# Kernel optimization log

Hardware: AMD Instinct MI355X
Metric: run time of the kernel (lower is better)

The kernel has to match this reference:

```python
import jax, jax.numpy as jnp
import numpy as np

N, E, D = 50000, 300000, 64
EPS = 0.0  # eps buffer, train_eps=False


def setup_inputs() -> dict:
    key = jax.random.key(0)
    ks = jax.random.split(key, 24)
    inp = {}
    i = 0
    for d in range(3):
        inp[f"x{d}"] = jax.random.normal(ks[i], (N, D), jnp.float32); i += 1
        inp[f"up_index{d}"] = jax.random.randint(ks[i], (2, E), 0, N, jnp.int32); i += 1
        inp[f"down_index{d}"] = jax.random.randint(ks[i], (2, E), 0, N, jnp.int32); i += 1
        inp[f"up_attr{d}"] = jax.random.normal(ks[i], (E, D), jnp.float32); i += 1
        inp[f"down_attr{d}"] = jax.random.normal(ks[i], (E, D), jnp.float32); i += 1
    s2 = 1.0 / np.sqrt(2 * D)
    s1 = 1.0 / np.sqrt(D)
    inp["W_up"] = jax.random.normal(ks[i], (2 * D, D), jnp.float32) * s2; i += 1
    inp["b_up"] = jnp.zeros((D,), jnp.float32)
    inp["W_down"] = jax.random.normal(ks[i], (2 * D, D), jnp.float32) * s2; i += 1
    inp["b_down"] = jnp.zeros((D,), jnp.float32)
    inp["W1"] = jax.random.normal(ks[i], (D, D), jnp.float32) * s1; i += 1
    inp["b1"] = jnp.zeros((D,), jnp.float32)
    inp["W2"] = jax.random.normal(ks[i], (D, D), jnp.float32) * s1; i += 1
    inp["b2"] = jnp.zeros((D,), jnp.float32)
    return inp


def _level(x, up_idx, down_idx, up_attr, down_attr,
           W_up, b_up, W_down, b_down, W1, b1, W2, b2):
    # message_up: gather source feats, concat attr, MLP, scatter-add to targets
    m_up = jax.nn.relu(jnp.concatenate([x[up_idx[1]], up_attr], axis=-1) @ W_up + b_up)
    out_up = jax.ops.segment_sum(m_up, up_idx[0], num_segments=N)
    m_dn = jax.nn.relu(jnp.concatenate([x[down_idx[1]], down_attr], axis=-1) @ W_down + b_down)
    out_dn = jax.ops.segment_sum(m_dn, down_idx[0], num_segments=N)
    # out_up += (1+eps)x; out_down += (1+eps)x; update(out_up + out_down)
    h = out_up + out_dn + (2.0 * (1.0 + EPS)) * x
    return jax.nn.relu(jax.nn.relu(h @ W1 + b1) @ W2 + b2)


def reference(x0, up_index0, down_index0, up_attr0, down_attr0,
              x1, up_index1, down_index1, up_attr1, down_attr1,
              x2, up_index2, down_index2, up_attr2, down_attr2,
              W_up, b_up, W_down, b_down, W1, b1, W2, b2):
    params = (W_up, b_up, W_down, b_down, W1, b1, W2, b2)
    o0 = _level(x0, up_index0, down_index0, up_attr0, down_attr0, *params)
    o1 = _level(x1, up_index1, down_index1, up_attr1, down_attr1, *params)
    o2 = _level(x2, up_index2, down_index2, up_attr2, down_attr2, *params)
    return (o0, o1, o2)
```

## Files before the change

kernel.cpp:

```cpp
#include <hip/hip_runtime.h>
#include <hip/hip_fp16.h>

#define NN 50000
#define NE 300000
#define ETILES (NE / 16)
#define NTILES (NN / 16)

typedef _Float16 f16;
typedef _Float16 f16x4 __attribute__((ext_vector_type(4)));
typedef float f32x4 __attribute__((ext_vector_type(4)));

__device__ __forceinline__ f16x4 cvt4(float4 v) {
    f16x4 r; r.x = (f16)v.x; r.y = (f16)v.y; r.z = (f16)v.z; r.w = (f16)v.w;
    return r;
}

template<bool HALF>
__global__ void init_kernel(const float* __restrict__ x0, const float* __restrict__ x1,
                            const float* __restrict__ x2, void* __restrict__ hbase) {
    const size_t i = (size_t)blockIdx.x * 256 + threadIdx.x;
    const int lvl = (int)(i / (NN * 16));
    const size_t li = i - (size_t)lvl * (NN * 16);
    const float* xs = (lvl == 0) ? x0 : (lvl == 1) ? x1 : x2;
    float4 v = ((const float4*)xs)[li];
    if (HALF) {
        f16x4 o;
        o.x = (f16)(2.f * v.x); o.y = (f16)(2.f * v.y);
        o.z = (f16)(2.f * v.z); o.w = (f16)(2.f * v.w);
        ((f16x4*)((f16*)hbase + (size_t)lvl * NN * 64))[li] = o;
    } else {
        ((float4*)((float*)hbase + (size_t)lvl * NN * 64))[li] =
            make_float4(2.f * v.x, 2.f * v.y, 2.f * v.z, 2.f * v.w);
    }
}

__global__ void wtrans_kernel(const float* __restrict__ WU, const float* __restrict__ WD,
                              f16* __restrict__ WtU, f16* __restrict__ WtD) {
    const int i = blockIdx.x * 256 + threadIdx.x;
    const int k = i >> 6, c = i & 63;
    WtU[c * 128 + k] = (f16)WU[i];
    WtD[c * 128 + k] = (f16)WD[i];
}

__global__ __launch_bounds__(256) void edge2_kernel(
    const float* __restrict__ x,
    const int* __restrict__ ui, const int* __restrict__ di,
    const float* __restrict__ ua, const float* __restrict__ da,
    const f16* __restrict__ WtU, const f16* __restrict__ WtD,
    const float* __restrict__ bU, const float* __restrict__ bD,
    __half* __restrict__ h) {

    const int dir = blockIdx.y;
    const int* __restrict__ idx   = dir ? di : ui;
    const float* __restrict__ attr = dir ? da : ua;
    const f16* __restrict__ Wt    = dir ? WtD : WtU;
    const float* __restrict__ b   = dir ? bD : bU;

    const int t    = threadIdx.x;
    const int lane = t & 63;
    const int wid  = t >> 6;
    const int lr   = lane & 15;
    const int lg   = (lane >> 4) & 3;
    const int l5   = lane & 31;

    f16x4 wf[8][4];
#pragma unroll
    for (int k0 = 0; k0 < 8; ++k0)
#pragma unroll
        for (int n = 0; n < 4; ++n)
            wf[k0][n] = *(const f16x4*)&Wt[(n * 16 + lr) * 128 + k0 * 16 + 4 * lg];
    float bf[4];
#pragma unroll
    for (int n = 0; n < 4; ++n) bf[n] = b[n * 16 + lr];

    const float4* x4 = (const float4*)x;
    const float4* a4 = (const float4*)attr;

    const int gw     = blockIdx.x * 4 + wid;
    const int stride = gridDim.x * 4;

    int tile = gw;
    if (tile >= ETILES) return;

    int comb;
    float4 pA[4];
    {
        const int e0 = tile << 4;
        comb = idx[(l5 < 16) ? (NE + e0 + l5) : (e0 + l5 - 16)];
#pragma unroll
        for (int k0 = 0; k0 < 4; ++k0)
            pA[k0] = a4[(size_t)(e0 + lr) * 16 + 4 * k0 + lg];
    }

    for (; tile < ETILES; tile += stride) {
        const int src = __shfl(comb, lr);
        int tg[4];
#pragma unroll
        for (int j = 0; j < 4; ++j) tg[j] = __shfl(comb, 16 + 4 * lg + j);

        float4 gx[4];
#pragma unroll
        for (int k0 = 0; k0 < 4; ++k0)
            gx[k0] = x4[(size_t)src * 16 + 4 * k0 + lg];

        const int tn = tile + stride;
        int combN = 0;
        float4 pAn[4] = {};
        if (tn < ETILES) {
            const int e0n = tn << 4;
            combN = idx[(l5 < 16) ? (NE + e0n + l5) : (e0n + l5 - 16)];
#pragma unroll
            for (int k0 = 0; k0 < 4; ++k0)
                pAn[k0] = a4[(size_t)(e0n + lr) * 16 + 4 * k0 + lg];
        }

        f16x4 a[8];
#pragma unroll
        for (int k0 = 0; k0 < 4; ++k0) a[4 + k0] = cvt4(pA[k0]);
#pragma unroll
        for (int k0 = 0; k0 < 4; ++k0) a[k0] = cvt4(gx[k0]);

        f32x4 acc[4];
#pragma unroll
        for (int n = 0; n < 4; ++n) acc[n] = (f32x4){0.f, 0.f, 0.f, 0.f};
#pragma unroll
        for (int k0 = 0; k0 < 8; ++k0)
#pragma unroll
            for (int n = 0; n < 4; ++n)
                acc[n] = __builtin_amdgcn_mfma_f32_16x16x16f16(a[k0], wf[k0][n], acc[n], 0, 0, 0);

#pragma unroll
        for (int j = 0; j < 4; ++j) {
            float v[4], vn[4];
#pragma unroll
            for (int n = 0; n < 4; ++n) v[n] = fmaxf(acc[n][j] + bf[n], 0.f);
#pragma unroll
            for (int n = 0; n < 4; ++n) vn[n] = __shfl_xor(v[n], 1);
            __half* hp = h + (size_t)tg[j] * 64;
            if ((lane & 1) == 0) {
                unsafeAtomicAdd((__half2*)(hp + 0 * 16 + lr), __floats2half2_rn(v[0], vn[0]));
                unsafeAtomicAdd((__half2*)(hp + 1 * 16 + lr), __floats2half2_rn(v[1], vn[1]));
            } else {
                unsafeAtomicAdd((__half2*)(hp + 2 * 16 + lr - 1), __floats2half2_rn(vn[2], v[2]));
                unsafeAtomicAdd((__half2*)(hp + 3 * 16 + lr - 1), __floats2half2_rn(vn[3], v[3]));
            }
        }

        comb = combN;
#pragma unroll
        for (int k0 = 0; k0 < 4; ++k0) pA[k0] = pAn[k0];
    }
}

__global__ __launch_bounds__(256) void edge_f32_kernel(
    const float* __restrict__ x, const int* __restrict__ idx,
    const float* __restrict__ attr, const float* __restrict__ W,
    const float* __restrict__ b, float* __restrict__ h) {

    const int t    = threadIdx.x;
    const int lane = t & 63;
    const int wid  = t >> 6;
    const int lr   = lane & 15;
    const int lg   = (lane >> 4) & 3;

    f16x4 wf[8][4];
#pragma unroll
    for (int k0 = 0; k0 < 8; ++k0) {
        const int kb = k0 * 16 + 4 * lg;
#pragma unroll
        for (int n = 0; n < 4; ++n) {
            const int c = n * 16 + lr;
            f16x4 w;
            w.x = (f16)W[(kb + 0) * 64 + c];
            w.y = (f16)W[(kb + 1) * 64 + c];
            w.z = (f16)W[(kb + 2) * 64 + c];
            w.w = (f16)W[(kb + 3) * 64 + c];
            wf[k0][n] = w;
        }
    }
    float bf[4];
#pragma unroll
    for (int n = 0; n < 4; ++n) bf[n] = b[n * 16 + lr];

    const float4* x4 = (const float4*)x;
    const float4* a4 = (const float4*)attr;

    const int gw     = blockIdx.x * 4 + wid;
    const int stride = gridDim.x * 4;
    for (int tile = gw; tile < ETILES; tile += stride) {
        const int e0  = tile << 4;
        const int src = idx[NE + e0 + lr];
        int tg[4];
#pragma unroll
        for (int j = 0; j < 4; ++j) tg[j] = idx[e0 + 4 * lg + j];

        f16x4 a[8];
#pragma unroll
        for (int k0 = 0; k0 < 4; ++k0)
            a[k0] = cvt4(x4[(size_t)src * 16 + 4 * k0 + lg]);
#pragma unroll
        for (int k0 = 0; k0 < 4; ++k0)
            a[4 + k0] = cvt4(a4[(size_t)(e0 + lr) * 16 + 4 * k0 + lg]);

        f32x4 acc[4];
#pragma unroll
        for (int n = 0; n < 4; ++n) acc[n] = (f32x4){0.f, 0.f, 0.f, 0.f};
#pragma unroll
        for (int k0 = 0; k0 < 8; ++k0)
#pragma unroll
            for (int n = 0; n < 4; ++n)
                acc[n] = __builtin_amdgcn_mfma_f32_16x16x16f16(a[k0], wf[k0][n], acc[n], 0, 0, 0);

#pragma unroll
        for (int j = 0; j < 4; ++j) {
            float* hp = h + (size_t)tg[j] * 64;
#pragma unroll
            for (int n = 0; n < 4; ++n) {
                float v = fmaxf(acc[n][j] + bf[n], 0.f);
                unsafeAtomicAdd(hp + n * 16 + lr, v);
            }
        }
    }
}

template<bool HALF>
__global__ __launch_bounds__(256) void node_kernel(
    const void* __restrict__ hbase, float* __restrict__ outb,
    const float* __restrict__ W1, const float* __restrict__ b1,
    const float* __restrict__ W2, const float* __restrict__ b2) {

    __shared__ f16 Y[4][16 * 72];

    const int t    = threadIdx.x;
    const int lane = t & 63;
    const int wid  = t >> 6;
    const int lr   = lane & 15;
    const int lg   = (lane >> 4) & 3;

    f16x4 w1f[4][4], w2f[4][4];
#pragma unroll
    for (int k0 = 0; k0 < 4; ++k0) {
        const int kb = k0 * 16 + 4 * lg;
#pragma unroll
        for (int n = 0; n < 4; ++n) {
            const int c = n * 16 + lr;
            f16x4 w;
            w.x = (f16)W1[(kb + 0) * 64 + c];
            w.y = (f16)W1[(kb + 1) * 64 + c];
            w.z = (f16)W1[(kb + 2) * 64 + c];
            w.w = (f16)W1[(kb + 3) * 64 + c];
            w1f[k0][n] = w;
            w.x = (f16)W2[(kb + 0) * 64 + c];
            w.y = (f16)W2[(kb + 1) * 64 + c];
            w.z = (f16)W2[(kb + 2) * 64 + c];
            w.w = (f16)W2[(kb + 3) * 64 + c];
            w2f[k0][n] = w;
        }
    }
    float b1f[4], b2f[4];
#pragma unroll
    for (int n = 0; n < 4; ++n) {
        b1f[n] = b1[n * 16 + lr];
        b2f[n] = b2[n * 16 + lr];
    }

    const int gw     = blockIdx.x * 4 + wid;
    const int stride = gridDim.x * 4;
    for (int tile = gw; tile < 3 * NTILES; tile += stride) {
        const int lvl = tile / NTILES;
        const int n0  = (tile - lvl * NTILES) << 4;
        float* out = outb + (size_t)lvl * NN * 64;

        f16x4 a[4];
        if (HALF) {
            const f16* h16 = (const f16*)hbase + (size_t)lvl * NN * 64;
#pragma unroll
            for (int k0 = 0; k0 < 4; ++k0)
                a[k0] = *(const f16x4*)&h16[(size_t)(n0 + lr) * 64 + k0 * 16 + 4 * lg];
        } else {
            const float4* h4 = (const float4*)((const float*)hbase + (size_t)lvl * NN * 64);
#pragma unroll
            for (int k0 = 0; k0 < 4; ++k0)
                a[k0] = cvt4(h4[(size_t)(n0 + lr) * 16 + 4 * k0 + lg]);
        }

        f32x4 acc[4];
#pragma unroll
        for (int n = 0; n < 4; ++n) acc[n] = (f32x4){0.f, 0.f, 0.f, 0.f};
#pragma unroll
        for (int k0 = 0; k0 < 4; ++k0)
#pragma unroll
            for (int n = 0; n < 4; ++n)
                acc[n] = __builtin_amdgcn_mfma_f32_16x16x16f16(a[k0], w1f[k0][n], acc[n], 0, 0, 0);

#pragma unroll
        for (int n = 0; n < 4; ++n)
#pragma unroll
            for (int j = 0; j < 4; ++j) {
                float v = acc[n][j] + b1f[n];
                v = v > 0.f ? v : 0.f;
                Y[wid][(4 * lg + j) * 72 + n * 16 + lr] = (f16)v;
            }

        f16x4 a2[4];
#pragma unroll
        for (int k0 = 0; k0 < 4; ++k0)
            a2[k0] = *(const f16x4*)&Y[wid][lr * 72 + k0 * 16 + 4 * lg];

        f32x4 acc2[4];
#pragma unroll
        for (int n = 0; n < 4; ++n) acc2[n] = (f32x4){0.f, 0.f, 0.f, 0.f};
#pragma unroll
        for (int k0 = 0; k0 < 4; ++k0)
#pragma unroll
            for (int n = 0; n < 4; ++n)
                acc2[n] = __builtin_amdgcn_mfma_f32_16x16x16f16(a2[k0], w2f[k0][n], acc2[n], 0, 0, 0);

#pragma unroll
        for (int n = 0; n < 4; ++n)
#pragma unroll
            for (int j = 0; j < 4; ++j) {
                float v = acc2[n][j] + b2f[n];
                v = v > 0.f ? v : 0.f;
                out[(size_t)(n0 + 4 * lg + j) * 64 + n * 16 + lr] = v;
            }
    }
}

extern "C" void kernel_launch(void* const* d_in, const int* in_sizes, int n_in,
                              void* d_out, int out_size, void* d_ws, size_t ws_size,
                              hipStream_t stream) {
    (void)in_sizes; (void)n_in; (void)out_size;

    const float* W_up   = (const float*)d_in[15];
    const float* b_up   = (const float*)d_in[16];
    const float* W_down = (const float*)d_in[17];
    const float* b_down = (const float*)d_in[18];
    const float* W1     = (const float*)d_in[19];
    const float* b1     = (const float*)d_in[20];
    const float* W2     = (const float*)d_in[21];
    const float* b2     = (const float*)d_in[22];

    const float* x0 = (const float*)d_in[0];
    const float* x1 = (const float*)d_in[5];
    const float* x2 = (const float*)d_in[10];

    const size_t hbytes = (size_t)3 * NN * 64 * sizeof(__half);
    const bool half_ok = ws_size >= hbytes + 2 * 128 * 64 * sizeof(f16);

    if (half_ok) {
        f16* hbase = (f16*)d_ws;
        f16* WtU = (f16*)((char*)d_ws + hbytes);
        f16* WtD = WtU + 128 * 64;

        wtrans_kernel<<<32, 256, 0, stream>>>(W_up, W_down, WtU, WtD);
        init_kernel<true><<<9375, 256, 0, stream>>>(x0, x1, x2, hbase);
        for (int d = 0; d < 3; ++d) {
            const float* x  = (const float*)d_in[5 * d + 0];
            const int*   ui = (const int*)  d_in[5 * d + 1];
            const int*   di = (const int*)  d_in[5 * d + 2];
            const float* ua = (const float*)d_in[5 * d + 3];
            const float* da = (const float*)d_in[5 * d + 4];
            __half* h = (__half*)(hbase + (size_t)d * NN * 64);
            edge2_kernel<<<dim3(1024, 2), 256, 0, stream>>>(
                x, ui, di, ua, da, WtU, WtD, b_up, b_down, h);
        }
        node_kernel<true><<<586, 256, 0, stream>>>(hbase, (float*)d_out, W1, b1, W2, b2);
    } else {
        float* hbase = (float*)d_out;
        init_kernel<false><<<9375, 256, 0, stream>>>(x0, x1, x2, hbase);
        for (int d = 0; d < 3; ++d) {
            const float* x  = (const float*)d_in[5 * d + 0];
            const int*   ui = (const int*)  d_in[5 * d + 1];
            const int*   di = (const int*)  d_in[5 * d + 2];
            const float* ua = (const float*)d_in[5 * d + 3];
            const float* da = (const float*)d_in[5 * d + 4];
            float* h = hbase + (size_t)d * NN * 64;
            edge_f32_kernel<<<1024, 256, 0, stream>>>(x, ui, ua, W_up,   b_up,   h);
            edge_f32_kernel<<<1024, 256, 0, stream>>>(x, di, da, W_down, b_down, h);
        }
        node_kernel<false><<<586, 256, 0, stream>>>(hbase, (float*)d_out, W1, b1, W2, b2);
    }
}
```

Before: 443.1 us.

## Gather fp16 copy of x, move weights to LDS, deepen edge prefetch pipeline

The init kernel now also writes an fp16 copy of each level's x, so the edge kernel gathers 128 bytes per row instead of 256. Weight fragments move from 32 VGPR-resident vectors into padded shared memory, which frees registers for occupancy and costs LDS reads per MFMA. The edge loop now prefetches indices two tiles ahead and gathered rows one tile ahead. The fp16 path needs a larger workspace; if the workspace is too small the code falls back to the fp32 path.

```diff
diff --git a/kernel.cpp b/kernel.cpp
--- a/kernel.cpp
+++ b/kernel.cpp
@@ -8,6 +8,7 @@
 
 typedef _Float16 f16;
 typedef _Float16 f16x4 __attribute__((ext_vector_type(4)));
+typedef _Float16 f16x8 __attribute__((ext_vector_type(8)));
 typedef float f32x4 __attribute__((ext_vector_type(4)));
 
 __device__ __forceinline__ f16x4 cvt4(float4 v) {
@@ -15,23 +16,30 @@
     return r;
 }
 
-template<bool HALF>
-__global__ void init_kernel(const float* __restrict__ x0, const float* __restrict__ x1,
-                            const float* __restrict__ x2, void* __restrict__ hbase) {
+__global__ void init2_kernel(const float* __restrict__ x0, const float* __restrict__ x1,
+                             const float* __restrict__ x2,
+                             f16* __restrict__ hbase, f16* __restrict__ xhbase) {
     const size_t i = (size_t)blockIdx.x * 256 + threadIdx.x;
     const int lvl = (int)(i / (NN * 16));
     const size_t li = i - (size_t)lvl * (NN * 16);
     const float* xs = (lvl == 0) ? x0 : (lvl == 1) ? x1 : x2;
     float4 v = ((const float4*)xs)[li];
-    if (HALF) {
-        f16x4 o;
-        o.x = (f16)(2.f * v.x); o.y = (f16)(2.f * v.y);
-        o.z = (f16)(2.f * v.z); o.w = (f16)(2.f * v.w);
-        ((f16x4*)((f16*)hbase + (size_t)lvl * NN * 64))[li] = o;
-    } else {
-        ((float4*)((float*)hbase + (size_t)lvl * NN * 64))[li] =
-            make_float4(2.f * v.x, 2.f * v.y, 2.f * v.z, 2.f * v.w);
-    }
+    f16x4 xo, ho;
+    xo.x = (f16)v.x;        xo.y = (f16)v.y;        xo.z = (f16)v.z;        xo.w = (f16)v.w;
+    ho.x = (f16)(2.f*v.x);  ho.y = (f16)(2.f*v.y);  ho.z = (f16)(2.f*v.z);  ho.w = (f16)(2.f*v.w);
+    ((f16x4*)(xhbase + (size_t)lvl * NN * 64))[li] = xo;
+    ((f16x4*)(hbase  + (size_t)lvl * NN * 64))[li] = ho;
+}
+
+__global__ void initf32_kernel(const float* __restrict__ x0, const float* __restrict__ x1,
+                               const float* __restrict__ x2, float* __restrict__ hbase) {
+    const size_t i = (size_t)blockIdx.x * 256 + threadIdx.x;
+    const int lvl = (int)(i / (NN * 16));
+    const size_t li = i - (size_t)lvl * (NN * 16);
+    const float* xs = (lvl == 0) ? x0 : (lvl == 1) ? x1 : x2;
+    float4 v = ((const float4*)xs)[li];
+    ((float4*)(hbase + (size_t)lvl * NN * 64))[li] =
+        make_float4(2.f * v.x, 2.f * v.y, 2.f * v.z, 2.f * v.w);
 }
 
 __global__ void wtrans_kernel(const float* __restrict__ WU, const float* __restrict__ WD,
@@ -42,92 +50,112 @@
     WtD[c * 128 + k] = (f16)WD[i];
 }
 
-__global__ __launch_bounds__(256) void edge2_kernel(
-    const float* __restrict__ x,
+#define WLDS_STRIDE 136
+
+__device__ __forceinline__ int ld_comb(const int* __restrict__ idx, int tile, int l5) {
+    const int e0 = tile << 4;
+    return idx[(l5 < 16) ? (NE + e0 + l5) : (e0 + l5 - 16)];
+}
+
+__global__ __launch_bounds__(256) void edge4_kernel(
+    const f16* __restrict__ xh,
     const int* __restrict__ ui, const int* __restrict__ di,
     const float* __restrict__ ua, const float* __restrict__ da,
     const f16* __restrict__ WtU, const f16* __restrict__ WtD,
     const float* __restrict__ bU, const float* __restrict__ bD,
     __half* __restrict__ h) {
 
+    __shared__ __align__(16) f16 Wlds[64 * WLDS_STRIDE];
+
     const int dir = blockIdx.y;
-    const int* __restrict__ idx   = dir ? di : ui;
+    const int* __restrict__ idx    = dir ? di : ui;
     const float* __restrict__ attr = dir ? da : ua;
-    const f16* __restrict__ Wt    = dir ? WtD : WtU;
-    const float* __restrict__ b   = dir ? bD : bU;
-
-    const int t    = threadIdx.x;
-    const int lane = t & 63;
-    const int wid  = t >> 6;
+    const f16* __restrict__ Wt     = dir ? WtD : WtU;
+    const float* __restrict__ b    = dir ? bD : bU;
+
+    const int tt   = threadIdx.x;
+    const int lane = tt & 63;
+    const int wid  = tt >> 6;
     const int lr   = lane & 15;
     const int lg   = (lane >> 4) & 3;
     const int l5   = lane & 31;
 
-    f16x4 wf[8][4];
-#pragma unroll
-    for (int k0 = 0; k0 < 8; ++k0)
-#pragma unroll
-        for (int n = 0; n < 4; ++n)
-            wf[k0][n] = *(const f16x4*)&Wt[(n * 16 + lr) * 128 + k0 * 16 + 4 * lg];
+    for (int i = tt; i < 1024; i += 256) {
+        const int row = i >> 4, seg = i & 15;
+        *(f16x8*)&Wlds[row * WLDS_STRIDE + seg * 8] = *(const f16x8*)&Wt[row * 128 + seg * 8];
+    }
     float bf[4];
 #pragma unroll
     for (int n = 0; n < 4; ++n) bf[n] = b[n * 16 + lr];
-
-    const float4* x4 = (const float4*)x;
+    __syncthreads();
+
     const float4* a4 = (const float4*)attr;
 
-    const int gw     = blockIdx.x * 4 + wid;
-    const int stride = gridDim.x * 4;
-
-    int tile = gw;
-    if (tile >= ETILES) return;
-
-    int comb;
+    const int S = gridDim.x * 4;
+    int t = blockIdx.x * 4 + wid;
+    if (t >= ETILES) return;
+
+    int cB;
+    int srcT, tgT[4];
+    f16x4 gx[4];
     float4 pA[4];
     {
-        const int e0 = tile << 4;
-        comb = idx[(l5 < 16) ? (NE + e0 + l5) : (e0 + l5 - 16)];
+        const int cA = ld_comb(idx, t, l5);
+        const int tn1 = t + S;
+        cB = ld_comb(idx, (tn1 < ETILES) ? tn1 : t, l5);
+        srcT = __shfl(cA, lr);
+#pragma unroll
+        for (int j = 0; j < 4; ++j) tgT[j] = __shfl(cA, 16 + 4 * lg + j);
+        const int e0 = t << 4;
+#pragma unroll
+        for (int k0 = 0; k0 < 4; ++k0)
+            gx[k0] = *(const f16x4*)&xh[(size_t)srcT * 64 + k0 * 16 + 4 * lg];
 #pragma unroll
         for (int k0 = 0; k0 < 4; ++k0)
             pA[k0] = a4[(size_t)(e0 + lr) * 16 + 4 * k0 + lg];
     }
 
-    for (; tile < ETILES; tile += stride) {
-        const int src = __shfl(comb, lr);
-        int tg[4];
-#pragma unroll
-        for (int j = 0; j < 4; ++j) tg[j] = __shfl(comb, 16 + 4 * lg + j);
-
-        float4 gx[4];
-#pragma unroll
-        for (int k0 = 0; k0 < 4; ++k0)
-            gx[k0] = x4[(size_t)src * 16 + 4 * k0 + lg];
-
-        const int tn = tile + stride;
-        int combN = 0;
-        float4 pAn[4] = {};
-        if (tn < ETILES) {
-            const int e0n = tn << 4;
-            combN = idx[(l5 < 16) ? (NE + e0n + l5) : (e0n + l5 - 16)];
+    for (; t < ETILES; t += S) {
+        const int tn  = t + S;
+        const int tnn = tn + S;
+
+        const int srcN = __shfl(cB, lr);
+        int tgN[4];
+#pragma unroll
+        for (int j = 0; j < 4; ++j) tgN[j] = __shfl(cB, 16 + 4 * lg + j);
+        const int cC = ld_comb(idx, (tnn < ETILES) ? tnn : t, l5);
+
+        const int tnc   = (tn < ETILES) ? tn : t;
+        const int srcNc = (tn < ETILES) ? srcN : srcT;
+        f16x4 gxN[4];
+        float4 pAN[4];
+        {
+            const int e0n = tnc << 4;
 #pragma unroll
             for (int k0 = 0; k0 < 4; ++k0)
-                pAn[k0] = a4[(size_t)(e0n + lr) * 16 + 4 * k0 + lg];
-        }
-
-        f16x4 a[8];
-#pragma unroll
-        for (int k0 = 0; k0 < 4; ++k0) a[4 + k0] = cvt4(pA[k0]);
-#pragma unroll
-        for (int k0 = 0; k0 < 4; ++k0) a[k0] = cvt4(gx[k0]);
+                gxN[k0] = *(const f16x4*)&xh[(size_t)srcNc * 64 + k0 * 16 + 4 * lg];
+#pragma unroll
+            for (int k0 = 0; k0 < 4; ++k0)
+                pAN[k0] = a4[(size_t)(e0n + lr) * 16 + 4 * k0 + lg];
+        }
+
+        f16x4 afr[8];
+#pragma unroll
+        for (int k0 = 0; k0 < 4; ++k0) afr[k0] = gx[k0];
+#pragma unroll
+        for (int k0 = 0; k0 < 4; ++k0) afr[4 + k0] = cvt4(pA[k0]);
 
         f32x4 acc[4];
 #pragma unroll
         for (int n = 0; n < 4; ++n) acc[n] = (f32x4){0.f, 0.f, 0.f, 0.f};
 #pragma unroll
-        for (int k0 = 0; k0 < 8; ++k0)
-#pragma unroll
-            for (int n = 0; n < 4; ++n)
-                acc[n] = __builtin_amdgcn_mfma_f32_16x16x16f16(a[k0], wf[k0][n], acc[n], 0, 0, 0);
+        for (int k0 = 0; k0 < 8; ++k0) {
+#pragma unroll
+            for (int n = 0; n < 4; ++n) {
+                const f16x4 wf = *(const f16x4*)&Wlds[(n * 16 + lr) * WLDS_STRIDE + k0 * 16 + 4 * lg];
+                acc[n] = __builtin_amdgcn_mfma_f32_16x16x16f16(afr[k0], wf, acc[n], 0, 0, 0);
+            }
+        }
 
 #pragma unroll
         for (int j = 0; j < 4; ++j) {
@@ -136,7 +164,7 @@
             for (int n = 0; n < 4; ++n) v[n] = fmaxf(acc[n][j] + bf[n], 0.f);
 #pragma unroll
             for (int n = 0; n < 4; ++n) vn[n] = __shfl_xor(v[n], 1);
-            __half* hp = h + (size_t)tg[j] * 64;
+            __half* hp = h + (size_t)tgT[j] * 64;
             if ((lane & 1) == 0) {
                 unsafeAtomicAdd((__half2*)(hp + 0 * 16 + lr), __floats2half2_rn(v[0], vn[0]));
                 unsafeAtomicAdd((__half2*)(hp + 1 * 16 + lr), __floats2half2_rn(v[1], vn[1]));
@@ -146,9 +174,12 @@
             }
         }
 
-        comb = combN;
-#pragma unroll
-        for (int k0 = 0; k0 < 4; ++k0) pA[k0] = pAn[k0];
+        srcT = srcN;
+#pragma unroll
+        for (int j = 0; j < 4; ++j) tgT[j] = tgN[j];
+#pragma unroll
+        for (int k0 = 0; k0 < 4; ++k0) { gx[k0] = gxN[k0]; pA[k0] = pAN[k0]; }
+        cB = cC;
     }
 }
 
@@ -345,30 +376,31 @@
     const float* x1 = (const float*)d_in[5];
     const float* x2 = (const float*)d_in[10];
 
-    const size_t hbytes = (size_t)3 * NN * 64 * sizeof(__half);
-    const bool half_ok = ws_size >= hbytes + 2 * 128 * 64 * sizeof(f16);
-
-    if (half_ok) {
-        f16* hbase = (f16*)d_ws;
-        f16* WtU = (f16*)((char*)d_ws + hbytes);
-        f16* WtD = WtU + 128 * 64;
+    const size_t hbytes  = (size_t)3 * NN * 64 * sizeof(f16);
+    const size_t need    = 2 * hbytes + (size_t)2 * 128 * 64 * sizeof(f16);
+
+    if (ws_size >= need) {
+        f16* hbase  = (f16*)d_ws;
+        f16* xhbase = hbase + (size_t)3 * NN * 64;
+        f16* WtU    = (f16*)((char*)d_ws + 2 * hbytes);
+        f16* WtD    = WtU + 128 * 64;
 
         wtrans_kernel<<<32, 256, 0, stream>>>(W_up, W_down, WtU, WtD);
-        init_kernel<true><<<9375, 256, 0, stream>>>(x0, x1, x2, hbase);
+        init2_kernel<<<9375, 256, 0, stream>>>(x0, x1, x2, hbase, xhbase);
         for (int d = 0; d < 3; ++d) {
-            const float* x  = (const float*)d_in[5 * d + 0];
             const int*   ui = (const int*)  d_in[5 * d + 1];
             const int*   di = (const int*)  d_in[5 * d + 2];
             const float* ua = (const float*)d_in[5 * d + 3];
             const float* da = (const float*)d_in[5 * d + 4];
+            const f16* xh = xhbase + (size_t)d * NN * 64;
             __half* h = (__half*)(hbase + (size_t)d * NN * 64);
-            edge2_kernel<<<dim3(1024, 2), 256, 0, stream>>>(
-                x, ui, di, ua, da, WtU, WtD, b_up, b_down, h);
+            edge4_kernel<<<dim3(1024, 2), 256, 0, stream>>>(
+                xh, ui, di, ua, da, WtU, WtD, b_up, b_down, h);
         }
         node_kernel<true><<<586, 256, 0, stream>>>(hbase, (float*)d_out, W1, b1, W2, b2);
     } else {
         float* hbase = (float*)d_out;
-        init_kernel<false><<<9375, 256, 0, stream>>>(x0, x1, x2, hbase);
+        initf32_kernel<<<9375, 256, 0, stream>>>(x0, x1, x2, hbase);
         for (int d = 0; d < 3; ++d) {
             const float* x  = (const float*)d_in[5 * d + 0];
             const int*   ui = (const int*)  d_in[5 * d + 1];
```

New measurement: 433.8 us. -2.1%, faster.
